# Kernel tuning notes

Measured on AMD Instinct MI355X. Metric: run time of the kernel, lower is better.

## Reference

```python
import jax, jax.numpy as jnp
import numpy as np

N_HEAD = 16
ROPE_THETA = 10000.0


def setup_inputs() -> dict:
    key = jax.random.key(0)
    k0, k1, k2 = jax.random.split(key, 3)
    B, T, C = 2, 2048, 1024
    s = 0.02  # GPT-2 style init scale
    return {
        "x": jax.random.normal(k0, (B, T, C), jnp.float32),
        "w_attn": jax.random.normal(k1, (C, 3 * C), jnp.float32) * s,
        "b_attn": jnp.zeros((3 * C,), jnp.float32),
        "w_proj": jax.random.normal(k2, (C, C), jnp.float32) * s,
        "b_proj": jnp.zeros((C,), jnp.float32),
    }


def _rope(x):
    # x: [B, H, T, D]; interleaved-pair rotary (lucidrains rotate_queries_or_keys)
    T, D = x.shape[-2], x.shape[-1]
    inv_freq = 1.0 / (ROPE_THETA ** (jnp.arange(0, D, 2, dtype=jnp.float32) / D))
    freqs = jnp.arange(T, dtype=jnp.float32)[:, None] * inv_freq[None, :]  # [T, D/2]
    emb = jnp.repeat(freqs, 2, axis=-1)  # [T, D], each freq duplicated per pair
    cos, sin = jnp.cos(emb), jnp.sin(emb)
    xr = x.reshape(*x.shape[:-1], D // 2, 2)
    x1, x2 = xr[..., 0], xr[..., 1]
    rot = jnp.stack((-x2, x1), axis=-1).reshape(x.shape)  # rotate_half
    return x * cos + rot * sin


def reference(x, w_attn, b_attn, w_proj, b_proj):
    B, T, C = x.shape
    H = N_HEAD
    D = C // H
    qkv = x @ w_attn + b_attn                      # [B, T, 3C]
    q, k, v = jnp.split(qkv, 3, axis=-1)

    def heads(t):
        return t.reshape(B, T, H, D).transpose(0, 2, 1, 3)  # [B, H, T, D]

    q, k, v = heads(q), heads(k), heads(v)
    q = _rope(q)
    k = _rope(k)

    att = jnp.einsum("bhqd,bhkd->bhqk", q, k) * (1.0 / np.sqrt(D))
    causal = jnp.tril(jnp.ones((T, T), dtype=bool))
    att = jnp.where(causal, att, -jnp.inf)
    att = jax.nn.softmax(att, axis=-1)
    y = jnp.einsum("bhqk,bhkd->bhqd", att, v)
    y = y.transpose(0, 2, 1, 3).reshape(B, T, C)
    return y @ w_proj + b_proj
```

## Files before the change

### kernel.cpp

```cpp
#include <hip/hip_runtime.h>
#include <hip/hip_bf16.h>
#include <stdint.h>

typedef __hip_bfloat16 bf16;
typedef __attribute__((ext_vector_type(8))) short bf16x8;
typedef __attribute__((ext_vector_type(4))) float f32x4;

__device__ inline float bf2f(bf16 v) { return __bfloat162float(v); }
__device__ inline bf16 f2bf(float f) { return __float2bfloat16(f); }

__device__ inline void glds16(const void* g, void* l) {
    __builtin_amdgcn_global_load_lds(
        (const __attribute__((address_space(1))) uint32_t*)g,
        (__attribute__((address_space(3))) uint32_t*)l, 16, 0, 0);
}

__global__ __launch_bounds__(256) void conv_x(const float* __restrict__ in,
                                              bf16* __restrict__ out)
{
    size_t i = ((size_t)blockIdx.x * 256 + threadIdx.x) * 8;
    float4 f0 = *(const float4*)(in + i);
    float4 f1 = *(const float4*)(in + i + 4);
    union { bf16x8 v; bf16 e[8]; } u;
    u.e[0] = f2bf(f0.x); u.e[1] = f2bf(f0.y); u.e[2] = f2bf(f0.z); u.e[3] = f2bf(f0.w);
    u.e[4] = f2bf(f1.x); u.e[5] = f2bf(f1.y); u.e[6] = f2bf(f1.z); u.e[7] = f2bf(f1.w);
    *(bf16x8*)(out + i) = u.v;
}

__global__ __launch_bounds__(256) void conv_wt(const float* __restrict__ W,
                                               bf16* __restrict__ Wt, int N, int K)
{
    __shared__ bf16 t[64][72];
    const int n0 = blockIdx.x * 64, k0 = blockIdx.y * 64;
    const int tid = threadIdx.x;
#pragma unroll
    for (int p = 0; p < 4; ++p) {
        int idx = p * 256 + tid;
        int kr = idx >> 4, c4 = idx & 15;
        float4 f = *(const float4*)(W + (size_t)(k0 + kr) * N + n0 + c4 * 4);
        t[kr][c4 * 4 + 0] = f2bf(f.x); t[kr][c4 * 4 + 1] = f2bf(f.y);
        t[kr][c4 * 4 + 2] = f2bf(f.z); t[kr][c4 * 4 + 3] = f2bf(f.w);
    }
    __syncthreads();
#pragma unroll
    for (int p = 0; p < 2; ++p) {
        int idx = p * 256 + tid;
        int nr = idx >> 3, ch = idx & 7;
        union { bf16x8 v; bf16 e[8]; } u;
#pragma unroll
        for (int j = 0; j < 8; ++j) u.e[j] = t[ch * 8 + j][nr];
        *(bf16x8*)(Wt + (size_t)(n0 + nr) * K + k0 + ch * 8) = u.v;
    }
}

template <bool OUTF32>
__global__ __launch_bounds__(256) void gemm_bt(
    const bf16* __restrict__ A, const bf16* __restrict__ Bt,
    const float* __restrict__ bias, int M, int N, int K, void* __restrict__ outv)
{
    __shared__ __align__(16) bf16 sa[128 * 32];
    __shared__ __align__(16) bf16 sb[128 * 32];

    const int tid  = threadIdx.x;
    const int wave = tid >> 6, lane = tid & 63;
    const int quad = lane >> 4, l16 = lane & 15;
    const int wm = wave >> 1, wn = wave & 1;
    const int row0 = blockIdx.x * 128, n0 = blockIdx.y * 128;

    f32x4 acc[4][4] = {};

    const int sm = wave * 16 + (lane >> 2);
    const int sk = (lane & 3) * 8;
    const bf16* ga = A  + (size_t)(row0 + sm) * K + sk;
    const bf16* gb = Bt + (size_t)(n0  + sm) * K + sk;
    bf16* la = sa + wave * 512;
    bf16* lb = sb + wave * 512;

    for (int k0 = 0; k0 < K; k0 += 32) {
        __syncthreads();
        glds16(ga + k0, la);
        glds16(ga + k0 + (size_t)64 * K, la + 2048);
        glds16(gb + k0, lb);
        glds16(gb + k0 + (size_t)64 * K, lb + 2048);
        __syncthreads();

        bf16x8 af[4], bfr[4];
#pragma unroll
        for (int mi = 0; mi < 4; ++mi)
            af[mi] = *(const bf16x8*)&sa[(wm * 64 + mi * 16 + l16) * 32 + quad * 8];
#pragma unroll
        for (int ni = 0; ni < 4; ++ni)
            bfr[ni] = *(const bf16x8*)&sb[(wn * 64 + ni * 16 + l16) * 32 + quad * 8];
#pragma unroll
        for (int mi = 0; mi < 4; ++mi)
#pragma unroll
            for (int ni = 0; ni < 4; ++ni)
                acc[mi][ni] = __builtin_amdgcn_mfma_f32_16x16x32_bf16(
                    af[mi], bfr[ni], acc[mi][ni], 0, 0, 0);
    }

#pragma unroll
    for (int ni = 0; ni < 4; ++ni) {
        int col = n0 + wn * 64 + ni * 16 + l16;
        float bvv = bias[col];
#pragma unroll
        for (int mi = 0; mi < 4; ++mi) {
#pragma unroll
            for (int r = 0; r < 4; ++r) {
                int row = row0 + wm * 64 + mi * 16 + quad * 4 + r;
                float v = acc[mi][ni][r] + bvv;
                if (OUTF32) ((float*)outv)[(size_t)row * N + col] = v;
                else        ((bf16*)outv)[(size_t)row * N + col] = f2bf(v);
            }
        }
    }
}

__global__ __launch_bounds__(256) void rope_k(
    const bf16* __restrict__ qkv, bf16* __restrict__ q, bf16* __restrict__ k)
{
    int gid = blockIdx.x * 256 + threadIdx.x;
    int p  = gid & 31, d0 = p * 2;
    int t  = (gid >> 5) & 2047;
    int h  = (gid >> 16) & 15;
    int b  = gid >> 20;

    size_t src = ((size_t)(b * 2048 + t)) * 3072 + h * 64 + d0;
    size_t dst = (((size_t)(b * 16 + h)) * 2048 + t) * 64 + d0;

    float invf = expf(-(float)d0 * (9.210340371976184f / 64.0f));
    float sn, cs;
    sincosf((float)t * invf, &sn, &cs);

    const float QS = 0.125f * 1.44269504088896f;
    float q0 = bf2f(qkv[src]),        q1 = bf2f(qkv[src + 1]);
    float k0 = bf2f(qkv[src + 1024]), k1 = bf2f(qkv[src + 1025]);
    q[dst]     = f2bf((q0 * cs - q1 * sn) * QS);
    q[dst + 1] = f2bf((q1 * cs + q0 * sn) * QS);
    k[dst]     = f2bf(k0 * cs - k1 * sn);
    k[dst + 1] = f2bf(k1 * cs + k0 * sn);
}

__global__ __launch_bounds__(256) void transpose_v(
    const bf16* __restrict__ qkv, bf16* __restrict__ vt)
{
    __shared__ bf16 t[64][72];
    const int t0 = blockIdx.x * 64;
    const int bh = blockIdx.y, b = bh >> 4, h = bh & 15;
    const int tid = threadIdx.x;
#pragma unroll
    for (int p = 0; p < 2; ++p) {
        int idx = p * 256 + tid;
        int tr = idx >> 3, ch = idx & 7;
        bf16x8 v = *(const bf16x8*)(qkv + ((size_t)(b * 2048 + t0 + tr)) * 3072
                                    + 2048 + h * 64 + ch * 8);
#pragma unroll
        for (int j = 0; j < 8; ++j) t[tr][ch * 8 + j] = ((const bf16*)&v)[j];
    }
    __syncthreads();
#pragma unroll
    for (int p = 0; p < 2; ++p) {
        int idx = p * 256 + tid;
        int dr = idx >> 3, ch = idx & 7;
        union { bf16x8 v; bf16 e[8]; } u;
#pragma unroll
        for (int j = 0; j < 8; ++j) u.e[j] = t[ch * 8 + j][dr];
        *(bf16x8*)(vt + ((size_t)bh * 64 + dr) * 2048 + t0 + ch * 8) = u.v;
    }
}

__global__ __launch_bounds__(256) void attn_k(
    const bf16* __restrict__ qg, const bf16* __restrict__ kg,
    const bf16* __restrict__ vtg, bf16* __restrict__ y)
{
    __shared__ __align__(16) bf16 sK[128 * 64];
    __shared__ __align__(16) bf16 sV[64 * 128];
    __shared__ __align__(16) bf16 pL[4][16][136];

    const int tid  = threadIdx.x;
    const int wave = tid >> 6, lane = tid & 63;
    const int quad = lane >> 4, l16 = lane & 15;
    const int bh   = blockIdx.x;
    const int qt   = 31 - (int)blockIdx.y;
    const bf16* Q  = qg  + (size_t)bh * 2048 * 64;
    const bf16* K  = kg  + (size_t)bh * 2048 * 64;
    const bf16* Vt = vtg + (size_t)bh * 64 * 2048;
    const int b = bh >> 4, h = bh & 15;

    const int q0 = qt * 64 + wave * 16;

    bf16x8 aq[2];
    aq[0] = *(const bf16x8*)(Q + (size_t)(q0 + l16) * 64 + quad * 8);
    aq[1] = *(const bf16x8*)(Q + (size_t)(q0 + l16) * 64 + 32 + quad * 8);

    union { bf16x8 v; short e[8]; } uo;
#pragma unroll
    for (int j = 0; j < 8; ++j) uo.e[j] = (short)0x3F80;
    const bf16x8 vones = uo.v;

    f32x4 o[4] = {};
    f32x4 ls   = {};
    float m_r[4] = {-1e30f, -1e30f, -1e30f, -1e30f};
    const float THR = 8.0f;

    for (int kt = 0; kt <= q0 + 15; kt += 128) {
        __syncthreads();
#pragma unroll
        for (int c = 0; c < 4; ++c) {
            int key = wave * 32 + c * 8 + (lane >> 3);
            int p = lane & 7;
            glds16(K + (size_t)(kt + key) * 64 + ((p ^ key) & 7) * 8,
                   &sK[(wave * 32 + c * 8) * 64]);
        }
#pragma unroll
        for (int c = 0; c < 4; ++c) {
            int d = wave * 16 + c * 4 + (lane >> 4);
            int p = lane & 15;
            glds16(Vt + (size_t)d * 2048 + kt + ((p ^ d) & 15) * 8,
                   &sV[(wave * 16 + c * 4) * 128]);
        }
        __syncthreads();

        const int nlast = min(7, (q0 - kt) >> 4);
        f32x4 sc[8];
        __builtin_amdgcn_s_setprio(1);
#pragma unroll
        for (int nt = 0; nt < 8; ++nt) {
            if (nt > nlast) continue;
            int key = nt * 16 + l16;
            f32x4 s0 = {};
            bf16x8 bk0 = *(const bf16x8*)&sK[key * 64 + ((quad ^ key) & 7) * 8];
            s0 = __builtin_amdgcn_mfma_f32_16x16x32_bf16(aq[0], bk0, s0, 0, 0, 0);
            bf16x8 bk1 = *(const bf16x8*)&sK[key * 64 + (((4 + quad) ^ key) & 7) * 8];
            sc[nt] = __builtin_amdgcn_mfma_f32_16x16x32_bf16(aq[1], bk1, s0, 0, 0, 0);
        }
        __builtin_amdgcn_s_setprio(0);
        {
            const int diag = (q0 - kt) >> 4;
            if (diag <= 7) {
                int key = kt + diag * 16 + l16;
#pragma unroll
                for (int r = 0; r < 4; ++r) {
                    int row = q0 + quad * 4 + r;
                    if (key > row) sc[diag][r] = -1e30f;
                }
            }
        }
        float rowmax[4] = {-1e30f, -1e30f, -1e30f, -1e30f};
#pragma unroll
        for (int nt = 0; nt < 8; ++nt) {
            if (nt > nlast) continue;
#pragma unroll
            for (int r = 0; r < 4; ++r) rowmax[r] = fmaxf(rowmax[r], sc[nt][r]);
        }
        bool okl = (rowmax[0] <= m_r[0] + THR) && (rowmax[1] <= m_r[1] + THR) &&
                   (rowmax[2] <= m_r[2] + THR) && (rowmax[3] <= m_r[3] + THR);
        if (!__all((int)okl)) {
#pragma unroll
            for (int off = 1; off < 16; off <<= 1)
#pragma unroll
                for (int r = 0; r < 4; ++r)
                    rowmax[r] = fmaxf(rowmax[r], __shfl_xor(rowmax[r], off));
            float alpha[4];
#pragma unroll
            for (int r = 0; r < 4; ++r) {
                float mn = fmaxf(m_r[r], rowmax[r]);
                alpha[r] = exp2f(m_r[r] - mn);
                m_r[r] = mn;
            }
#pragma unroll
            for (int nt = 0; nt < 4; ++nt)
#pragma unroll
                for (int r = 0; r < 4; ++r) o[nt][r] *= alpha[r];
#pragma unroll
            for (int r = 0; r < 4; ++r) ls[r] *= alpha[r];
        }
#pragma unroll
        for (int nt = 0; nt < 8; ++nt) {
            if (nt > nlast) continue;
#pragma unroll
            for (int r = 0; r < 4; ++r) sc[nt][r] = exp2f(sc[nt][r] - m_r[r]);
        }

#pragma unroll
        for (int nt = 0; nt < 8; ++nt) {
            if (nt > nlast) continue;
            int blk = (2 * nt + (l16 >> 3)) ^ quad;
#pragma unroll
            for (int r = 0; r < 4; ++r)
                pL[wave][quad * 4 + r][blk * 8 + (l16 & 7)] = f2bf(sc[nt][r]);
        }
        if (nlast < 7 && !(nlast & 1)) {
            int blk = (2 * (nlast + 1) + (l16 >> 3)) ^ quad;
#pragma unroll
            for (int r = 0; r < 4; ++r)
                pL[wave][quad * 4 + r][blk * 8 + (l16 & 7)] = f2bf(0.f);
        }
        __builtin_amdgcn_s_setprio(1);
#pragma unroll
        for (int c = 0; c < 4; ++c) {
            if (c > (nlast >> 1)) continue;
            bf16x8 pa = *(const bf16x8*)&pL[wave][l16][(((4 * c + quad) ^ (l16 >> 2)) * 8)];
            ls = __builtin_amdgcn_mfma_f32_16x16x32_bf16(pa, vones, ls, 0, 0, 0);
#pragma unroll
            for (int dnt = 0; dnt < 4; ++dnt) {
                int d = dnt * 16 + l16;
                int cc = c * 4 + quad;
                bf16x8 vb = *(const bf16x8*)&sV[d * 128 + ((cc ^ d) & 15) * 8];
                o[dnt] = __builtin_amdgcn_mfma_f32_16x16x32_bf16(pa, vb, o[dnt], 0, 0, 0);
            }
        }
        __builtin_amdgcn_s_setprio(0);
    }

#pragma unroll
    for (int r = 0; r < 4; ++r) {
        float inv = 1.0f / ls[r];
        int qq = q0 + quad * 4 + r;
#pragma unroll
        for (int nt = 0; nt < 4; ++nt) {
            int d = nt * 16 + l16;
            y[((size_t)(b * 2048 + qq)) * 1024 + h * 64 + d] = f2bf(o[nt][r] * inv);
        }
    }
}

extern "C" void kernel_launch(void* const* d_in, const int* in_sizes, int n_in,
                              void* d_out, int out_size, void* d_ws, size_t ws_size,
                              hipStream_t stream) {
    const float* x      = (const float*)d_in[0];
    const float* w_attn = (const float*)d_in[1];
    const float* b_attn = (const float*)d_in[2];
    const float* w_proj = (const float*)d_in[3];
    const float* b_proj = (const float*)d_in[4];
    float* out = (float*)d_out;

    bf16* xbf = (bf16*)d_ws;
    bf16* wat = xbf + (size_t)4194304;
    bf16* wpt = wat + (size_t)3145728;
    bf16* qkv = wpt + (size_t)1048576;
    bf16* qh  = qkv + (size_t)12582912;
    bf16* kh  = qh  + (size_t)4194304;
    bf16* vt  = kh  + (size_t)4194304;
    bf16* yws = vt  + (size_t)4194304;

    dim3 blk(256);
    conv_x<<<dim3(2048), blk, 0, stream>>>(x, xbf);
    conv_wt<<<dim3(48, 16), blk, 0, stream>>>(w_attn, wat, 3072, 1024);
    conv_wt<<<dim3(16, 16), blk, 0, stream>>>(w_proj, wpt, 1024, 1024);
    gemm_bt<false><<<dim3(32, 24), blk, 0, stream>>>(xbf, wat, b_attn,
                                                     4096, 3072, 1024, qkv);
    rope_k<<<dim3(8192), blk, 0, stream>>>(qkv, qh, kh);
    transpose_v<<<dim3(32, 32), blk, 0, stream>>>(qkv, vt);
    attn_k<<<dim3(32, 32), blk, 0, stream>>>(qh, kh, vt, yws);
    gemm_bt<true><<<dim3(32, 8), blk, 0, stream>>>(yws, wpt, b_proj,
                                                   4096, 1024, 1024, out);
    (void)in_sizes; (void)n_in; (void)ws_size; (void)out_size;
}
```

Baseline: 226.2 us.

## Fuse RoPE into QKV GEMM epilogue with precomputed trig table

```diff
diff --git a/kernel.cpp b/kernel.cpp
--- a/kernel.cpp
+++ b/kernel.cpp
@@ -53,6 +53,16 @@
     }
 }
 
+__global__ __launch_bounds__(256) void trig_tab(float2* __restrict__ tab)
+{
+    int gid = blockIdx.x * 256 + threadIdx.x;
+    int p = gid & 31, t = gid >> 5;
+    float invf = expf(-(float)(2 * p) * (9.210340371976184f / 64.0f));
+    float sn, cs;
+    sincosf((float)t * invf, &sn, &cs);
+    tab[gid] = make_float2(cs, sn);
+}
+
 template <bool OUTF32>
 __global__ __launch_bounds__(256) void gemm_bt(
     const bf16* __restrict__ A, const bf16* __restrict__ Bt,
@@ -116,33 +126,88 @@
     }
 }
 
-__global__ __launch_bounds__(256) void rope_k(
-    const bf16* __restrict__ qkv, bf16* __restrict__ q, bf16* __restrict__ k)
-{
-    int gid = blockIdx.x * 256 + threadIdx.x;
-    int p  = gid & 31, d0 = p * 2;
-    int t  = (gid >> 5) & 2047;
-    int h  = (gid >> 16) & 15;
-    int b  = gid >> 20;
-
-    size_t src = ((size_t)(b * 2048 + t)) * 3072 + h * 64 + d0;
-    size_t dst = (((size_t)(b * 16 + h)) * 2048 + t) * 64 + d0;
-
-    float invf = expf(-(float)d0 * (9.210340371976184f / 64.0f));
-    float sn, cs;
-    sincosf((float)t * invf, &sn, &cs);
+__global__ __launch_bounds__(256) void gemm_qkv(
+    const bf16* __restrict__ A, const bf16* __restrict__ Bt,
+    const float* __restrict__ bias, const float2* __restrict__ tab,
+    bf16* __restrict__ qh, bf16* __restrict__ kh, bf16* __restrict__ vc)
+{
+    const int M = 4096, N = 3072, K = 1024;
+    __shared__ __align__(16) bf16 sa[128 * 32];
+    __shared__ __align__(16) bf16 sb[128 * 32];
+
+    const int tid  = threadIdx.x;
+    const int wave = tid >> 6, lane = tid & 63;
+    const int quad = lane >> 4, l16 = lane & 15;
+    const int wm = wave >> 1, wn = wave & 1;
+    const int row0 = blockIdx.x * 128, n0 = blockIdx.y * 128;
+
+    f32x4 acc[4][4] = {};
+
+    const int sm = wave * 16 + (lane >> 2);
+    const int sk = (lane & 3) * 8;
+    const bf16* ga = A  + (size_t)(row0 + sm) * K + sk;
+    const bf16* gb = Bt + (size_t)(n0  + sm) * K + sk;
+    bf16* la = sa + wave * 512;
+    bf16* lb = sb + wave * 512;
+
+    for (int k0 = 0; k0 < K; k0 += 32) {
+        __syncthreads();
+        glds16(ga + k0, la);
+        glds16(ga + k0 + (size_t)64 * K, la + 2048);
+        glds16(gb + k0, lb);
+        glds16(gb + k0 + (size_t)64 * K, lb + 2048);
+        __syncthreads();
+
+        bf16x8 af[4], bfr[4];
+#pragma unroll
+        for (int mi = 0; mi < 4; ++mi)
+            af[mi] = *(const bf16x8*)&sa[(wm * 64 + mi * 16 + l16) * 32 + quad * 8];
+#pragma unroll
+        for (int ni = 0; ni < 4; ++ni)
+            bfr[ni] = *(const bf16x8*)&sb[(wn * 64 + ni * 16 + l16) * 32 + quad * 8];
+#pragma unroll
+        for (int mi = 0; mi < 4; ++mi)
+#pragma unroll
+            for (int ni = 0; ni < 4; ++ni)
+                acc[mi][ni] = __builtin_amdgcn_mfma_f32_16x16x32_bf16(
+                    af[mi], bfr[ni], acc[mi][ni], 0, 0, 0);
+    }
 
     const float QS = 0.125f * 1.44269504088896f;
-    float q0 = bf2f(qkv[src]),        q1 = bf2f(qkv[src + 1]);
-    float k0 = bf2f(qkv[src + 1024]), k1 = bf2f(qkv[src + 1025]);
-    q[dst]     = f2bf((q0 * cs - q1 * sn) * QS);
-    q[dst + 1] = f2bf((q1 * cs + q0 * sn) * QS);
-    k[dst]     = f2bf(k0 * cs - k1 * sn);
-    k[dst + 1] = f2bf(k1 * cs + k0 * sn);
+#pragma unroll
+    for (int ni = 0; ni < 4; ++ni) {
+        int col = n0 + wn * 64 + ni * 16 + l16;
+        float bvv = bias[col];
+        int sec = col >> 10;
+        int cd  = col & 1023;
+        int h   = cd >> 6, d = cd & 63;
+        int p   = d >> 1;
+        bool odd = (d & 1) != 0;
+#pragma unroll
+        for (int mi = 0; mi < 4; ++mi) {
+#pragma unroll
+            for (int r = 0; r < 4; ++r) {
+                int row = row0 + wm * 64 + mi * 16 + quad * 4 + r;
+                float v = acc[mi][ni][r] + bvv;
+                float vp = __shfl_xor(v, 1);
+                if (sec == 2) {
+                    vc[(size_t)row * 1024 + cd] = f2bf(v);
+                } else {
+                    int tt = row & 2047, b = row >> 11;
+                    float2 cssn = tab[tt * 32 + p];
+                    float ro = odd ? (v * cssn.x + vp * cssn.y)
+                                   : (v * cssn.x - vp * cssn.y);
+                    size_t dst = (((size_t)(b * 16 + h)) * 2048 + tt) * 64 + d;
+                    if (sec == 0) qh[dst] = f2bf(ro * QS);
+                    else          kh[dst] = f2bf(ro);
+                }
+            }
+        }
+    }
 }
 
 __global__ __launch_bounds__(256) void transpose_v(
-    const bf16* __restrict__ qkv, bf16* __restrict__ vt)
+    const bf16* __restrict__ vc, bf16* __restrict__ vt)
 {
     __shared__ bf16 t[64][72];
     const int t0 = blockIdx.x * 64;
@@ -152,8 +217,8 @@
     for (int p = 0; p < 2; ++p) {
         int idx = p * 256 + tid;
         int tr = idx >> 3, ch = idx & 7;
-        bf16x8 v = *(const bf16x8*)(qkv + ((size_t)(b * 2048 + t0 + tr)) * 3072
-                                    + 2048 + h * 64 + ch * 8);
+        bf16x8 v = *(const bf16x8*)(vc + ((size_t)(b * 2048 + t0 + tr)) * 1024
+                                    + h * 64 + ch * 8);
 #pragma unroll
         for (int j = 0; j < 8; ++j) t[tr][ch * 8 + j] = ((const bf16*)&v)[j];
     }
@@ -338,20 +403,20 @@
     bf16* xbf = (bf16*)d_ws;
     bf16* wat = xbf + (size_t)4194304;
     bf16* wpt = wat + (size_t)3145728;
-    bf16* qkv = wpt + (size_t)1048576;
-    bf16* qh  = qkv + (size_t)12582912;
+    float2* tab = (float2*)(wpt + (size_t)1048576);
+    bf16* qh  = wpt + (size_t)1048576 + 262144;
     bf16* kh  = qh  + (size_t)4194304;
-    bf16* vt  = kh  + (size_t)4194304;
+    bf16* vc  = kh  + (size_t)4194304;
+    bf16* vt  = vc  + (size_t)4194304;
     bf16* yws = vt  + (size_t)4194304;
 
     dim3 blk(256);
     conv_x<<<dim3(2048), blk, 0, stream>>>(x, xbf);
     conv_wt<<<dim3(48, 16), blk, 0, stream>>>(w_attn, wat, 3072, 1024);
     conv_wt<<<dim3(16, 16), blk, 0, stream>>>(w_proj, wpt, 1024, 1024);
-    gemm_bt<false><<<dim3(32, 24), blk, 0, stream>>>(xbf, wat, b_attn,
-                                                     4096, 3072, 1024, qkv);
-    rope_k<<<dim3(8192), blk, 0, stream>>>(qkv, qh, kh);
-    transpose_v<<<dim3(32, 32), blk, 0, stream>>>(qkv, vt);
+    trig_tab<<<dim3(256), blk, 0, stream>>>(tab);
+    gemm_qkv<<<dim3(32, 24), blk, 0, stream>>>(xbf, wat, b_attn, tab, qh, kh, vc);
+    transpose_v<<<dim3(32, 32), blk, 0, stream>>>(vc, vt);
     attn_k<<<dim3(32, 32), blk, 0, stream>>>(qh, kh, vt, yws);
     gemm_bt<true><<<dim3(32, 8), blk, 0, stream>>>(yws, wpt, b_proj,
                                                    4096, 1024, 1024, out);
```

After: 228.6 us. No clear change (+1.1%).
